# Kernel optimization log

Measured on AMD Instinct MI355X. Metric: run time of the kernel, lower is better.

Reference implementation:

```python
import jax, jax.numpy as jnp
import numpy as np

DIM_KERNSIZE = 9           # taps per side = ceil(9/2) = 5
LAB_SCALE = (100.0, 254.0, 254.0)
INPUT_SIZE_FACTOR = 1.0    # IndexHelper.input_size_factor() assumed 1.0 (resolution-relative scalar)


def _bilinear_sample(img, offs):
    """Sample img [bs,C,H,W] at normalized uv = pixel_center_uv + offs.
    offs: [bs,T,2,H,W] (channel 0 = x/u, channel 1 = y/v). Border-clamped bilinear
    (torch.grid_sample align_corners=False, padding_mode='border').
    Returns [bs,T,C,H,W]."""
    bs, C, H, W = img.shape
    T = offs.shape[1]
    base_u = ((jnp.arange(W, dtype=img.dtype) + 0.5) / W)[None, None, None, :]
    base_v = ((jnp.arange(H, dtype=img.dtype) + 0.5) / H)[None, None, :, None]
    u = offs[:, :, 0] + base_u                 # [bs,T,H,W]
    v = offs[:, :, 1] + base_v
    xp = u * W - 0.5                           # continuous pixel coords
    yp = v * H - 0.5
    x0 = jnp.floor(xp)
    y0 = jnp.floor(yp)
    fx = (xp - x0)[:, :, None]                 # [bs,T,1,H,W]
    fy = (yp - y0)[:, :, None]
    x0i = jnp.clip(x0.astype(jnp.int32), 0, W - 1)
    x1i = jnp.clip(x0.astype(jnp.int32) + 1, 0, W - 1)
    y0i = jnp.clip(y0.astype(jnp.int32), 0, H - 1)
    y1i = jnp.clip(y0.astype(jnp.int32) + 1, 0, H - 1)
    flat = img.reshape(bs, C, H * W)

    def gather(yi, xi):
        lin = (yi * W + xi).reshape(bs, 1, T * H * W)          # broadcast over C
        vals = jnp.take_along_axis(flat, lin, axis=2)          # [bs,C,T*H*W]
        return vals.reshape(bs, C, T, H, W).transpose(0, 2, 1, 3, 4)

    v00 = gather(y0i, x0i)
    v01 = gather(y0i, x1i)
    v10 = gather(y1i, x0i)
    v11 = gather(y1i, x1i)
    top = v00 * (1.0 - fx) + v01 * fx
    bot = v10 * (1.0 - fx) + v11 * fx
    return top * (1.0 - fy) + bot * fy


def _bilateral_forward(x, tangent, sigmaD, sigmaR):
    bs, C, H, W = x.shape
    eps = jnp.finfo(x.dtype).eps
    # u_pass=True: direction along the tangent field
    direction_full = tangent                                   # [bs,2,H,W]
    max_extend = jnp.max(jnp.abs(direction_full), axis=1)      # [bs,H,W]
    ds = jnp.where(max_extend > 0, 1.0 / max_extend, jnp.ones_like(max_extend))
    tex = jnp.array([W, H], dtype=x.dtype).reshape(1, 2, 1, 1)
    direction = direction_full / tex                           # uv step per unit tap
    sD = sigmaD.reshape(bs, 1, 1, 1, 1) * INPUT_SIZE_FACTOR
    sR = sigmaR.reshape(bs, 1, 1, 1, 1)
    two_sD2 = 2.0 * sD * sD
    two_sR2 = 2.0 * sR * sR
    half_step = 2.0 * sD

    it1 = jnp.arange(1, DIM_KERNSIZE + 1, 2, dtype=x.dtype).reshape(1, -1, 1, 1, 1)
    it2 = jnp.arange(2, DIM_KERNSIZE + 2, 2, dtype=x.dtype).reshape(1, -1, 1, 1, 1)
    dsv = ds[:, None, None]                                    # [bs,1,1,H,W]
    itr1 = dsv * it1                                           # [bs,T,1,H,W]
    itr2 = dsv * it2

    def gk(t, two_s2):
        return jnp.exp(-t * t / (two_s2 + eps))

    kD1 = gk(itr1, two_sD2)
    kD2 = gk(itr2, two_sD2)
    kernelD = jnp.where(jnp.abs(itr1) <= half_step, kD1 + kD2, jnp.zeros_like(kD1))
    itr_d = (itr1 * kD1 + itr2 * kD2) / (kernelD + eps)        # merged tap position

    offs = itr_d * direction[:, None]                          # [bs,T,2,H,W]
    c0 = _bilinear_sample(x, offs)                             # [bs,T,C,H,W]
    c1 = _bilinear_sample(x, -offs)

    # guide is None -> g0=c0, g1=c1, guide=x
    scale = jnp.array(LAB_SCALE, dtype=x.dtype).reshape(1, 1, 3, 1, 1)
    cc0 = (c0 - x[:, None]) * scale
    cc1 = (c1 - x[:, None]) * scale
    tiny = jnp.asarray(1e-30, x.dtype)  # grad-safe sqrt; forward change negligible
    e0 = jnp.sqrt(jnp.maximum(jnp.sum(cc0 * cc0, axis=2, keepdims=True), tiny))
    e1 = jnp.sqrt(jnp.maximum(jnp.sum(cc1 * cc1, axis=2, keepdims=True), tiny))
    kE0 = gk(e0, two_sR2)
    kE1 = gk(e1, two_sR2)

    norm = 1.0 + jnp.sum(kernelD * kE0, axis=1) + jnp.sum(kernelD * kE1, axis=1)   # [bs,1,H,W]
    acc = x + jnp.sum(kernelD * kE0 * c0, axis=1) + jnp.sum(kernelD * kE1 * c1, axis=1)
    return acc / norm


def setup_inputs() -> dict:
    key = jax.random.key(0)
    k1, k2, k3, k4 = jax.random.split(key, 4)
    bs, C, H, W = 2, 3, 768, 1024
    x = jax.random.uniform(k1, (bs, C, H, W), dtype=jnp.float32)
    tangent = jax.random.normal(k2, (bs, 2, H, W), dtype=jnp.float32)
    sigmaD = jax.random.uniform(k3, (bs,), dtype=jnp.float32) * 4.0 + 2.0   # ~2..6 px
    sigmaR = jax.random.uniform(k4, (bs,), dtype=jnp.float32) * 10.0 + 5.0  # Lab-scale range sigma
    return {"x": x, "tangent": tangent, "sigmaD": sigmaD, "sigmaR": sigmaR}


def reference(x, tangent, sigmaD, sigmaR):
    return _bilateral_forward(x, tangent, sigmaD, sigmaR)
```

## Files before the change

### kernel.cpp

```cpp
#include <hip/hip_runtime.h>
#include <hip/hip_fp16.h>
#include <math.h>

#define HH 768
#define WW 1024
#define HW (HH * WW)
#define NTAPS 5
#define F_EPS 1.1920929e-07f
#define LOG2E 1.44269504f

#define TS   32
#define RAD  10
#define ROWS 53
#define COLS 53
#define TP   54

typedef __fp16 h2 __attribute__((ext_vector_type(2)));
typedef float  f2 __attribute__((ext_vector_type(2)));
union H2U { h2 h; unsigned u; };

__device__ __forceinline__ float fast_rcp(float v) {
    return __builtin_amdgcn_rcpf(v);
}
__device__ __forceinline__ h2 as_h2(unsigned u) { H2U t; t.u = u; return t.h; }

__global__ __launch_bounds__(1024, 2) void fab_tile(
    const float* __restrict__ x,
    const float* __restrict__ tangent,
    const float* __restrict__ sigmaD,
    const float* __restrict__ sigmaR,
    float* __restrict__ out)
{
    __shared__ uint2 tileT[ROWS * TP];

    const int tiles_x = WW / TS;
    const int tiles_y = HH / TS;
    const int tpb = tiles_x * tiles_y;
    int tid = threadIdx.x;
    int bid = blockIdx.x;
    int b = bid / tpb;
    int tq = bid - b * tpb;
    int tyi = tq / tiles_x;
    int txi = tq - tyi * tiles_x;
    int tx0 = txi * TS, ty0 = tyi * TS;

    const float* xb = x + (size_t)b * 3 * HW;

    for (int cI = tid; cI < ROWS * COLS; cI += 1024) {
        int syy = cI / COLS;
        int sxx = cI - syy * COLS;
        int wx = tx0 - RAD + sxx;
        int sgx  = min(max(wx, 0), WW - 1);
        int sgx1 = min(max(wx + 1, 0), WW - 1);
        int sgy = min(max(ty0 - RAD + syy, 0), HH - 1);
        int g = sgy * WW;
        float a0v = xb[g + sgx]  * 100.0f;
        float a1v = xb[g + sgx1] * 100.0f;
        float c1v = xb[HW + g + sgx]     * 254.0f;
        float c2v = xb[2 * HW + g + sgx] * 254.0f;
        H2U pa; pa.h = __builtin_amdgcn_cvt_pkrtz(a0v, a1v);
        H2U pb; pb.h = __builtin_amdgcn_cvt_pkrtz(c1v, c2v);
        uint2 v; v.x = pa.u; v.y = pb.u;
        tileT[syy * TP + sxx] = v;
    }
    __syncthreads();

    int lx = tid & (TS - 1);
    int ly = tid >> 5;
    int w = tx0 + lx, h = ty0 + ly;
    int p = h * WW + w;

    float tx = tangent[(size_t)b * 2 * HW + p];
    float ty = tangent[(size_t)b * 2 * HW + HW + p];
    float me = fmaxf(fabsf(tx), fabsf(ty));
    float ds = (me > 0.0f) ? fast_rcp(me) : 1.0f;
    float sD = sigmaD[b], sR = sigmaR[b];
    float half_step = 2.0f * sD;
    float nD = -fast_rcp(2.0f * sD * sD + F_EPS) * LOG2E;
    float nR = -fast_rcp(2.0f * sR * sR + F_EPS) * LOG2E;

    float C0 = xb[p] * 100.0f;
    float C1 = xb[HW + p] * 254.0f;
    float C2 = xb[2 * HW + p] * 254.0f;

    const f2 C0p = {C0, C0};
    const f2 C1p = {C1, C1};
    const f2 C2p = {C2, C2};
    const f2 nR2 = {nR, nR};

    f2 normp = {0.0f, 0.0f};
    f2 a0p = {0.0f, 0.0f};
    f2 a1p = {0.0f, 0.0f};
    f2 a2p = {0.0f, 0.0f};

    int ibase_a = (RAD + ly) * TP + (RAD + lx);
    int ibase_b = ibase_a - TP - 1;

    float Q  = __builtin_amdgcn_exp2f(ds * ds * nD);
    float Q2 = Q * Q;
    float pw = Q;
    float rq = Q2 * Q;

    const unsigned* td = (const unsigned*)tileT;

#pragma unroll
    for (int t = 0; t < NTAPS; ++t) {
        float itr1 = ds * (float)(2 * t + 1);
        float itr2 = ds * (float)(2 * t + 2);
        float kD1 = pw; pw *= rq; rq *= Q2;
        float kD2 = pw; pw *= rq; rq *= Q2;
        if (itr1 > half_step) continue;
        float kernelD = kD1 + kD2;
        float itr_d = (itr1 * kD1 + itr2 * kD2) * fast_rcp(kernelD + F_EPS);
        float ox = itr_d * tx;
        float oy = itr_d * ty;

        float fox = floorf(ox), foy = floorf(oy);
        float f_x = ox - fox,   f_y = oy - foy;
        int iox = (int)fox, ioy = (int)foy;
        int d = ioy * TP + iox;
        int i0a = ibase_a + d;
        int i0b = ibase_b - d;

        uint2 Ta  = tileT[i0a];
        uint2 Tta = tileT[i0a + TP];
        unsigned Bra = td[2 * i0a + 3];
        unsigned Bba = td[2 * i0a + 2 * TP + 3];
        uint2 Tb  = tileT[i0b];
        uint2 Ttb = tileT[i0b + TP];
        unsigned Brb = td[2 * i0b + 3];
        unsigned Bbb = td[2 * i0b + 2 * TP + 3];

        float gxa = 1.0f - f_x, gya = 1.0f - f_y;
        float w00 = gxa * gya, w01 = f_x * gya, w10 = gxa * f_y, w11 = f_x * f_y;
        h2 Wt  = __builtin_amdgcn_cvt_pkrtz(w00, w01);
        h2 Wb  = __builtin_amdgcn_cvt_pkrtz(w10, w11);
        h2 WtR = __builtin_shufflevector(Wb, Wb, 1, 0);
        h2 WbR = __builtin_shufflevector(Wt, Wt, 1, 0);
        h2 W00 = __builtin_amdgcn_cvt_pkrtz(w00, w00);
        h2 W01 = __builtin_amdgcn_cvt_pkrtz(w01, w01);
        h2 W10 = __builtin_amdgcn_cvt_pkrtz(w10, w10);
        h2 W11 = __builtin_amdgcn_cvt_pkrtz(w11, w11);

        h2 m0a = as_h2(Ta.x) * Wt + as_h2(Tta.x) * Wb;
        float s0a = (float)m0a.x + (float)m0a.y;
        h2 s12a = W00 * as_h2(Ta.y) + W01 * as_h2(Bra)
                + W10 * as_h2(Tta.y) + W11 * as_h2(Bba);

        h2 m0b = as_h2(Tb.x) * WtR + as_h2(Ttb.x) * WbR;
        float s0b = (float)m0b.x + (float)m0b.y;
        h2 s12b = W11 * as_h2(Tb.y) + W10 * as_h2(Brb)
                + W01 * as_h2(Ttb.y) + W00 * as_h2(Bbb);

        f2 s0p = {s0a, s0b};
        f2 s1p = {(float)s12a.x, (float)s12b.x};
        f2 s2p = {(float)s12a.y, (float)s12b.y};

        f2 cc0 = s0p - C0p;
        f2 cc1 = s1p - C1p;
        f2 cc2 = s2p - C2p;
        f2 e2p = cc0 * cc0 + cc1 * cc1 + cc2 * cc2;
        f2 e2n = e2p * nR2;
        f2 kEp = {__builtin_amdgcn_exp2f(e2n.x), __builtin_amdgcn_exp2f(e2n.y)};
        f2 kDp = {kernelD, kernelD};
        f2 wgtp = kEp * kDp;
        normp += wgtp;
        a0p += wgtp * s0p;
        a1p += wgtp * s1p;
        a2p += wgtp * s2p;
    }

    float norm = 1.0f + normp.x + normp.y;
    float a0 = C0 + a0p.x + a0p.y;
    float a1 = C1 + a1p.x + a1p.y;
    float a2 = C2 + a2p.x + a2p.y;

    float inv = fast_rcp(norm);
    size_t ob = (size_t)b * 3 * HW;
    out[ob + p]          = a0 * inv * 0.01f;
    out[ob + HW + p]     = a1 * inv * (1.0f / 254.0f);
    out[ob + 2 * HW + p] = a2 * inv * (1.0f / 254.0f);
}

extern "C" void kernel_launch(void* const* d_in, const int* in_sizes, int n_in,
                              void* d_out, int out_size, void* d_ws, size_t ws_size,
                              hipStream_t stream) {
    const float* x = (const float*)d_in[0];
    const float* tangent = (const float*)d_in[1];
    const float* sigmaD = (const float*)d_in[2];
    const float* sigmaR = (const float*)d_in[3];
    float* out = (float*)d_out;

    int bs = in_sizes[2];
    int tpb = (WW / TS) * (HH / TS);
    fab_tile<<<bs * tpb, 1024, 0, stream>>>(x, tangent, sigmaD, sigmaR, out);
}
```

Baseline: 31.66 us.

## Process two pixels per thread with taller 32x64 tiles and packed bilinear weights

Enlarges each block's tile to 32x64 pixels so every thread handles two rows. This amortizes the halo load into shared memory: 85 rows are staged for 64 output rows instead of 53 rows for 32. The four bilinear weights are now built with packed half multiplies of x and y weight pairs rather than eight separate conversions. It also drops the min-2-blocks launch bound, which may change register allocation and occupancy. Halving the block count (384 blocks) risks poorer load balance across CUs.

```diff
diff --git a/kernel.cpp b/kernel.cpp
--- a/kernel.cpp
+++ b/kernel.cpp
@@ -9,10 +9,11 @@
 #define F_EPS 1.1920929e-07f
 #define LOG2E 1.44269504f
 
-#define TS   32
+#define TSX  32
+#define TSY  64
 #define RAD  10
-#define ROWS 53
 #define COLS 53
+#define ROWS 85
 #define TP   54
 
 typedef __fp16 h2 __attribute__((ext_vector_type(2)));
@@ -23,8 +24,10 @@
     return __builtin_amdgcn_rcpf(v);
 }
 __device__ __forceinline__ h2 as_h2(unsigned u) { H2U t; t.u = u; return t.h; }
+#define SH(v,i)    __builtin_shufflevector((v), (v), (i), (i))
+#define SWAP2(v)   __builtin_shufflevector((v), (v), 1, 0)
 
-__global__ __launch_bounds__(1024, 2) void fab_tile(
+__global__ __launch_bounds__(1024) void fab_tile(
     const float* __restrict__ x,
     const float* __restrict__ tangent,
     const float* __restrict__ sigmaD,
@@ -33,8 +36,8 @@
 {
     __shared__ uint2 tileT[ROWS * TP];
 
-    const int tiles_x = WW / TS;
-    const int tiles_y = HH / TS;
+    const int tiles_x = WW / TSX;
+    const int tiles_y = HH / TSY;
     const int tpb = tiles_x * tiles_y;
     int tid = threadIdx.x;
     int bid = blockIdx.x;
@@ -42,7 +45,7 @@
     int tq = bid - b * tpb;
     int tyi = tq / tiles_x;
     int txi = tq - tyi * tiles_x;
-    int tx0 = txi * TS, ty0 = tyi * TS;
+    int tx0 = txi * TSX, ty0 = tyi * TSY;
 
     const float* xb = x + (size_t)b * 3 * HW;
 
@@ -65,121 +68,119 @@
     }
     __syncthreads();
 
-    int lx = tid & (TS - 1);
-    int ly = tid >> 5;
-    int w = tx0 + lx, h = ty0 + ly;
-    int p = h * WW + w;
-
-    float tx = tangent[(size_t)b * 2 * HW + p];
-    float ty = tangent[(size_t)b * 2 * HW + HW + p];
-    float me = fmaxf(fabsf(tx), fabsf(ty));
-    float ds = (me > 0.0f) ? fast_rcp(me) : 1.0f;
+    int lx = tid & (TSX - 1);
+    int ly0 = tid >> 5;
     float sD = sigmaD[b], sR = sigmaR[b];
     float half_step = 2.0f * sD;
     float nD = -fast_rcp(2.0f * sD * sD + F_EPS) * LOG2E;
     float nR = -fast_rcp(2.0f * sR * sR + F_EPS) * LOG2E;
-
-    float C0 = xb[p] * 100.0f;
-    float C1 = xb[HW + p] * 254.0f;
-    float C2 = xb[2 * HW + p] * 254.0f;
-
-    const f2 C0p = {C0, C0};
-    const f2 C1p = {C1, C1};
-    const f2 C2p = {C2, C2};
     const f2 nR2 = {nR, nR};
-
-    f2 normp = {0.0f, 0.0f};
-    f2 a0p = {0.0f, 0.0f};
-    f2 a1p = {0.0f, 0.0f};
-    f2 a2p = {0.0f, 0.0f};
-
-    int ibase_a = (RAD + ly) * TP + (RAD + lx);
-    int ibase_b = ibase_a - TP - 1;
-
-    float Q  = __builtin_amdgcn_exp2f(ds * ds * nD);
-    float Q2 = Q * Q;
-    float pw = Q;
-    float rq = Q2 * Q;
-
     const unsigned* td = (const unsigned*)tileT;
 
 #pragma unroll
-    for (int t = 0; t < NTAPS; ++t) {
-        float itr1 = ds * (float)(2 * t + 1);
-        float itr2 = ds * (float)(2 * t + 2);
-        float kD1 = pw; pw *= rq; rq *= Q2;
-        float kD2 = pw; pw *= rq; rq *= Q2;
-        if (itr1 > half_step) continue;
-        float kernelD = kD1 + kD2;
-        float itr_d = (itr1 * kD1 + itr2 * kD2) * fast_rcp(kernelD + F_EPS);
-        float ox = itr_d * tx;
-        float oy = itr_d * ty;
+    for (int q = 0; q < 2; ++q) {
+        int ly = ly0 + q * 32;
+        int w = tx0 + lx, h = ty0 + ly;
+        int p = h * WW + w;
 
-        float fox = floorf(ox), foy = floorf(oy);
-        float f_x = ox - fox,   f_y = oy - foy;
-        int iox = (int)fox, ioy = (int)foy;
-        int d = ioy * TP + iox;
-        int i0a = ibase_a + d;
-        int i0b = ibase_b - d;
+        float tx = tangent[(size_t)b * 2 * HW + p];
+        float ty = tangent[(size_t)b * 2 * HW + HW + p];
+        float me = fmaxf(fabsf(tx), fabsf(ty));
+        float ds = (me > 0.0f) ? fast_rcp(me) : 1.0f;
 
-        uint2 Ta  = tileT[i0a];
-        uint2 Tta = tileT[i0a + TP];
-        unsigned Bra = td[2 * i0a + 3];
-        unsigned Bba = td[2 * i0a + 2 * TP + 3];
-        uint2 Tb  = tileT[i0b];
-        uint2 Ttb = tileT[i0b + TP];
-        unsigned Brb = td[2 * i0b + 3];
-        unsigned Bbb = td[2 * i0b + 2 * TP + 3];
+        float C0 = xb[p] * 100.0f;
+        float C1 = xb[HW + p] * 254.0f;
+        float C2 = xb[2 * HW + p] * 254.0f;
+        const f2 C0p = {C0, C0};
+        const f2 C1p = {C1, C1};
+        const f2 C2p = {C2, C2};
 
-        float gxa = 1.0f - f_x, gya = 1.0f - f_y;
-        float w00 = gxa * gya, w01 = f_x * gya, w10 = gxa * f_y, w11 = f_x * f_y;
-        h2 Wt  = __builtin_amdgcn_cvt_pkrtz(w00, w01);
-        h2 Wb  = __builtin_amdgcn_cvt_pkrtz(w10, w11);
-        h2 WtR = __builtin_shufflevector(Wb, Wb, 1, 0);
-        h2 WbR = __builtin_shufflevector(Wt, Wt, 1, 0);
-        h2 W00 = __builtin_amdgcn_cvt_pkrtz(w00, w00);
-        h2 W01 = __builtin_amdgcn_cvt_pkrtz(w01, w01);
-        h2 W10 = __builtin_amdgcn_cvt_pkrtz(w10, w10);
-        h2 W11 = __builtin_amdgcn_cvt_pkrtz(w11, w11);
+        f2 normp = {0.0f, 0.0f};
+        f2 a0p = {0.0f, 0.0f};
+        f2 a1p = {0.0f, 0.0f};
+        f2 a2p = {0.0f, 0.0f};
 
-        h2 m0a = as_h2(Ta.x) * Wt + as_h2(Tta.x) * Wb;
-        float s0a = (float)m0a.x + (float)m0a.y;
-        h2 s12a = W00 * as_h2(Ta.y) + W01 * as_h2(Bra)
-                + W10 * as_h2(Tta.y) + W11 * as_h2(Bba);
+        int ibase_a = (RAD + ly) * TP + (RAD + lx);
+        int ibase_b = ibase_a - TP - 1;
 
-        h2 m0b = as_h2(Tb.x) * WtR + as_h2(Ttb.x) * WbR;
-        float s0b = (float)m0b.x + (float)m0b.y;
-        h2 s12b = W11 * as_h2(Tb.y) + W10 * as_h2(Brb)
-                + W01 * as_h2(Ttb.y) + W00 * as_h2(Bbb);
+        float Q  = __builtin_amdgcn_exp2f(ds * ds * nD);
+        float Q2 = Q * Q;
+        float pw = Q;
+        float rq = Q2 * Q;
 
-        f2 s0p = {s0a, s0b};
-        f2 s1p = {(float)s12a.x, (float)s12b.x};
-        f2 s2p = {(float)s12a.y, (float)s12b.y};
+#pragma unroll
+        for (int t = 0; t < NTAPS; ++t) {
+            float itr1 = ds * (float)(2 * t + 1);
+            float itr2 = ds * (float)(2 * t + 2);
+            float kD1 = pw; pw *= rq; rq *= Q2;
+            float kD2 = pw; pw *= rq; rq *= Q2;
+            if (itr1 > half_step) continue;
+            float kernelD = kD1 + kD2;
+            float itr_d = (itr1 * kD1 + itr2 * kD2) * fast_rcp(kernelD + F_EPS);
+            float ox = itr_d * tx;
+            float oy = itr_d * ty;
 
-        f2 cc0 = s0p - C0p;
-        f2 cc1 = s1p - C1p;
-        f2 cc2 = s2p - C2p;
-        f2 e2p = cc0 * cc0 + cc1 * cc1 + cc2 * cc2;
-        f2 e2n = e2p * nR2;
-        f2 kEp = {__builtin_amdgcn_exp2f(e2n.x), __builtin_amdgcn_exp2f(e2n.y)};
-        f2 kDp = {kernelD, kernelD};
-        f2 wgtp = kEp * kDp;
-        normp += wgtp;
-        a0p += wgtp * s0p;
-        a1p += wgtp * s1p;
-        a2p += wgtp * s2p;
+            float fox = floorf(ox), foy = floorf(oy);
+            float f_x = ox - fox,   f_y = oy - foy;
+            int iox = (int)fox, ioy = (int)foy;
+            int d = ioy * TP + iox;
+            int i0a = ibase_a + d;
+            int i0b = ibase_b - d;
+
+            uint2 Ta  = tileT[i0a];
+            uint2 Tta = tileT[i0a + TP];
+            unsigned Bra = td[2 * i0a + 3];
+            unsigned Bba = td[2 * i0a + 2 * TP + 3];
+            uint2 Tb  = tileT[i0b];
+            uint2 Ttb = tileT[i0b + TP];
+            unsigned Brb = td[2 * i0b + 3];
+            unsigned Bbb = td[2 * i0b + 2 * TP + 3];
+
+            float gxa = 1.0f - f_x, gya = 1.0f - f_y;
+            h2 Wx = __builtin_amdgcn_cvt_pkrtz(gxa, f_x);
+            h2 Wy = __builtin_amdgcn_cvt_pkrtz(gya, f_y);
+            h2 Wt = Wx * SH(Wy, 0);
+            h2 Wb = Wx * SH(Wy, 1);
+
+            h2 m0a = as_h2(Ta.x) * Wt + as_h2(Tta.x) * Wb;
+            float s0a = (float)m0a.x + (float)m0a.y;
+            h2 s12a = as_h2(Ta.y)  * SH(Wt, 0) + as_h2(Bra) * SH(Wt, 1)
+                    + as_h2(Tta.y) * SH(Wb, 0) + as_h2(Bba) * SH(Wb, 1);
+
+            h2 m0b = as_h2(Tb.x) * SWAP2(Wb) + as_h2(Ttb.x) * SWAP2(Wt);
+            float s0b = (float)m0b.x + (float)m0b.y;
+            h2 s12b = as_h2(Tb.y)  * SH(Wb, 1) + as_h2(Brb) * SH(Wb, 0)
+                    + as_h2(Ttb.y) * SH(Wt, 1) + as_h2(Bbb) * SH(Wt, 0);
+
+            f2 s0p = {s0a, s0b};
+            f2 s1p = {(float)s12a.x, (float)s12b.x};
+            f2 s2p = {(float)s12a.y, (float)s12b.y};
+
+            f2 cc0 = s0p - C0p;
+            f2 cc1 = s1p - C1p;
+            f2 cc2 = s2p - C2p;
+            f2 e2p = cc0 * cc0 + cc1 * cc1 + cc2 * cc2;
+            f2 e2n = e2p * nR2;
+            f2 kEp = {__builtin_amdgcn_exp2f(e2n.x), __builtin_amdgcn_exp2f(e2n.y)};
+            f2 kDp = {kernelD, kernelD};
+            f2 wgtp = kEp * kDp;
+            normp += wgtp;
+            a0p += wgtp * s0p;
+            a1p += wgtp * s1p;
+            a2p += wgtp * s2p;
+        }
+
+        float norm = 1.0f + normp.x + normp.y;
+        float a0 = C0 + a0p.x + a0p.y;
+        float a1 = C1 + a1p.x + a1p.y;
+        float a2 = C2 + a2p.x + a2p.y;
+
+        float inv = fast_rcp(norm);
+        size_t ob = (size_t)b * 3 * HW;
+        out[ob + p]          = a0 * inv * 0.01f;
+        out[ob + HW + p]     = a1 * inv * (1.0f / 254.0f);
+        out[ob + 2 * HW + p] = a2 * inv * (1.0f / 254.0f);
     }
-
-    float norm = 1.0f + normp.x + normp.y;
-    float a0 = C0 + a0p.x + a0p.y;
-    float a1 = C1 + a1p.x + a1p.y;
-    float a2 = C2 + a2p.x + a2p.y;
-
-    float inv = fast_rcp(norm);
-    size_t ob = (size_t)b * 3 * HW;
-    out[ob + p]          = a0 * inv * 0.01f;
-    out[ob + HW + p]     = a1 * inv * (1.0f / 254.0f);
-    out[ob + 2 * HW + p] = a2 * inv * (1.0f / 254.0f);
 }
 
 extern "C" void kernel_launch(void* const* d_in, const int* in_sizes, int n_in,
@@ -192,6 +193,6 @@
     float* out = (float*)d_out;
 
     int bs = in_sizes[2];
-    int tpb = (WW / TS) * (HH / TS);
+    int tpb = (WW / TSX) * (HH / TSY);
     fab_tile<<<bs * tpb, 1024, 0, stream>>>(x, tangent, sigmaD, sigmaR, out);
 }
```

Result: slower. 32.39 us (+2.3%).
